# Performance work log

Measured on AMD Instinct MI355X. Metric: run time of the kernel, lower is better.

Reference implementation:

```python
import jax, jax.numpy as jnp
import numpy as np
from jax import lax

NUM_HEADS = 8
RATIO_H = 2
RATIO_W = 2


def _layer_norm(x, gamma, beta, eps=1e-5):
    mean = jnp.mean(x, axis=-1, keepdims=True)
    var = jnp.var(x, axis=-1, keepdims=True)
    return (x - mean) * lax.rsqrt(var + eps) * gamma + beta


def setup_inputs() -> dict:
    key = jax.random.key(0)
    ks = jax.random.split(key, 6)
    B, N, C = 4, 4096, 512
    std = 0.02
    return {
        "x": jax.random.normal(ks[0], (B, N, C), jnp.float32),
        "w_qkv": jax.random.normal(ks[1], (3 * C, C), jnp.float32) * std,
        "w_ke": jax.random.normal(ks[2], (C, C, RATIO_H, RATIO_W), jnp.float32) * std,
        "w_ve": jax.random.normal(ks[3], (C, C, RATIO_H, RATIO_W), jnp.float32) * std,
        "gamma_k": jnp.ones((C // NUM_HEADS,), jnp.float32),
        "beta_k": jnp.zeros((C // NUM_HEADS,), jnp.float32),
        "gamma_v": jnp.ones((C // NUM_HEADS,), jnp.float32),
        "beta_v": jnp.zeros((C // NUM_HEADS,), jnp.float32),
        "w_proj": jax.random.normal(ks[4], (C, C), jnp.float32) * std,
        "b_proj": jnp.zeros((C,), jnp.float32),
    }


def reference(x, w_qkv, w_ke, w_ve, gamma_k, beta_k, gamma_v, beta_v, w_proj, b_proj):
    B, N, C = x.shape
    H = W = int(np.sqrt(N))
    h = NUM_HEADS
    hd = C // h
    s = RATIO_H * RATIO_W
    scale = hd ** -0.5

    # qkv projection (no bias): [B, N, 3C]
    qkv = jnp.einsum('bnc,dc->bnd', x, w_qkv)
    q, k, v = jnp.split(qkv, 3, axis=-1)

    # q -> [B, h, N, hd]
    q = q.reshape(B, N, h, hd).transpose(0, 2, 1, 3)

    # spatial reduction of k, v via strided conv (kernel == stride, no bias)
    def reduce_kv(t, w):
        img = t.transpose(0, 2, 1).reshape(B, C, H, W)
        red = lax.conv_general_dilated(
            img, w, window_strides=(RATIO_H, RATIO_W), padding='VALID',
            dimension_numbers=('NCHW', 'OIHW', 'NCHW'))  # [B, C, H/rh, W/rw]
        return red.reshape(B, C, N // s).transpose(0, 2, 1).reshape(
            B, N // s, h, hd).transpose(0, 2, 1, 3)  # [B, h, N/s, hd]

    k = _layer_norm(reduce_kv(k, w_ke), gamma_k, beta_k)
    v = _layer_norm(reduce_kv(v, w_ve), gamma_v, beta_v)

    # attention: [B, h, N, N/s]
    attn = jax.nn.softmax(jnp.einsum('bhqd,bhkd->bhqk', q, k) * scale, axis=-1)
    out = jnp.einsum('bhqk,bhkd->bhqd', attn, v)  # [B, h, N, hd]
    out = out.transpose(0, 2, 1, 3).reshape(B, N, C)
    return jnp.einsum('bnc,dc->bnd', out, w_proj) + b_proj
```

## Files before the change

### kernel.cpp

```cpp
#include <hip/hip_runtime.h>
#include <hip/hip_bf16.h>

#define DEVI static __device__ __forceinline__

typedef __attribute__((ext_vector_type(4))) float f32x4;
typedef __attribute__((ext_vector_type(8))) short bf16x8;
typedef __attribute__((ext_vector_type(4))) short s16x4;
typedef __attribute__((ext_vector_type(2))) unsigned int u32x2;

DEVI unsigned short f2bf(float f) {
    union { float f; unsigned u; } v; v.f = f;
    unsigned r = v.u + 0x7fffu + ((v.u >> 16) & 1u);
    return (unsigned short)(r >> 16);
}

DEVI void gload_lds16(const void* g, void* l) {
    __builtin_amdgcn_global_load_lds(
        (const __attribute__((address_space(1))) unsigned int*)(g),
        (__attribute__((address_space(3))) unsigned int*)(l), 16, 0, 0);
}

#define EXP2A(d, x) asm("v_exp_f32 %0, %1" : "=v"(d) : "v"(x))
#define CVTPK(d, a, b) asm("v_cvt_pk_bf16_f32 %0, %1, %2" : "=v"(d) : "v"(a), "v"(b))

__global__ __launch_bounds__(256) void prep_kernel(
    const float* __restrict__ x, const float* __restrict__ w_qkv,
    const float* __restrict__ w_proj, const float* __restrict__ w_ke,
    const float* __restrict__ w_ve,
    unsigned short* __restrict__ xb, unsigned short* __restrict__ wqkvb,
    unsigned short* __restrict__ wprojb, unsigned short* __restrict__ w2k,
    unsigned short* __restrict__ w2v, unsigned short* __restrict__ wqkvT)
{
    const int blk = blockIdx.x, t = threadIdx.x;
    if (blk < 9216) {
        const float* src; unsigned short* dst; int i;
        if (blk < 8192)      { src = x;      dst = xb;     i = (blk * 256 + t) * 4; }
        else if (blk < 8960) { src = w_qkv;  dst = wqkvb;  i = ((blk - 8192) * 256 + t) * 4; }
        else                 { src = w_proj; dst = wprojb; i = ((blk - 8960) * 256 + t) * 4; }
        const float4 v = *(const float4*)(src + i);
        ushort4 o; o.x = f2bf(v.x); o.y = f2bf(v.y); o.z = f2bf(v.z); o.w = f2bf(v.w);
        *(ushort4*)(dst + i) = o;
    } else if (blk < 11264) {
        const int r = blk - 9216;
        const float* wsrc = (r < 1024) ? w_ke : w_ve;
        unsigned short* wdst = (r < 1024) ? w2k : w2v;
        const int i4 = (((r & 1023) * 256) + t) * 4;
        const int o = i4 >> 11, p = (i4 >> 9) & 3, c = i4 & 511;
        const float* s = wsrc + (o << 11) + (c << 2) + p;
        ushort4 ov; ov.x = f2bf(s[0]); ov.y = f2bf(s[4]); ov.z = f2bf(s[8]); ov.w = f2bf(s[12]);
        *(ushort4*)(wdst + i4) = ov;
    } else {
        const int r2 = blk - 11264;
        const int i4 = (r2 * 256 + t) * 4;
        const int sel = i4 >> 18;
        const int rem = i4 & 262143;
        const int d = rem >> 9, c4 = rem & 511;
        const float* s = w_qkv + (size_t)(512 + sel * 512 + c4) * 512 + d;
        ushort4 ov; ov.x = f2bf(s[0]); ov.y = f2bf(s[512]); ov.z = f2bf(s[1024]); ov.w = f2bf(s[1536]);
        *(ushort4*)(wqkvT + i4) = ov;
    }
}

template<int OUT_BF16, int ADD_BIAS>
__global__ __launch_bounds__(256) void gemm_bt(
    const unsigned short* __restrict__ A,
    const unsigned short* __restrict__ B,
    void* __restrict__ Cp, const float* __restrict__ bias,
    int N, int K)
{
    __shared__ unsigned short As[128 * 64];
    __shared__ unsigned short Bs[128 * 64];
    const int t = threadIdx.x;
    const int lane = t & 63, w = t >> 6;
    const int wr = w >> 1, wc = w & 1;
    const int lr = lane & 15, lg = lane >> 4;
    const size_t rowBase = (size_t)blockIdx.y * 128;
    const size_t colBase = (size_t)blockIdx.x * 128;

    const unsigned short* gA[4]; const unsigned short* gB[4]; int du[4];
#pragma unroll
    for (int j = 0; j < 4; ++j) {
        const int u = t * 16 + j * 4096;
        const int row = u >> 7, colb = u & 127;
        const int csw = colb ^ ((row & 7) << 4);
        du[j] = u;
        gA[j] = A + (rowBase + row) * (size_t)K + (csw >> 1);
        gB[j] = B + (colBase + row) * (size_t)K + (csw >> 1);
    }
    const int sw = (lr & 7) << 4;

    f32x4 acc[4][4] = {};

    for (int k0 = 0; k0 < K; k0 += 64) {
#pragma unroll
        for (int j = 0; j < 4; ++j) {
            gload_lds16(gA[j] + k0, (char*)As + du[j]);
            gload_lds16(gB[j] + k0, (char*)Bs + du[j]);
        }
        __syncthreads();
#pragma unroll
        for (int s = 0; s < 2; ++s) {
            const int ro = (s * 64 + lg * 16) ^ sw;
            bf16x8 af[4], bfr[4];
#pragma unroll
            for (int a = 0; a < 4; ++a)
                af[a] = *(const bf16x8*)((char*)As + (wr * 64 + a * 16 + lr) * 128 + ro);
#pragma unroll
            for (int bn = 0; bn < 4; ++bn)
                bfr[bn] = *(const bf16x8*)((char*)Bs + (wc * 64 + bn * 16 + lr) * 128 + ro);
#pragma unroll
            for (int a = 0; a < 4; ++a)
#pragma unroll
                for (int bn = 0; bn < 4; ++bn)
                    acc[a][bn] = __builtin_amdgcn_mfma_f32_16x16x32_bf16(af[a], bfr[bn], acc[a][bn], 0, 0, 0);
        }
        __syncthreads();
    }

#pragma unroll
    for (int a = 0; a < 4; ++a) {
        const size_t row = rowBase + wr * 64 + a * 16 + lg * 4;
#pragma unroll
        for (int bn = 0; bn < 4; ++bn) {
            const size_t col = colBase + wc * 64 + bn * 16 + lr;
#pragma unroll
            for (int r = 0; r < 4; ++r) {
                const float v = acc[a][bn][r];
                if (OUT_BF16) {
                    ((unsigned short*)Cp)[(row + r) * (size_t)N + col] = f2bf(v);
                } else {
                    const float vb2 = ADD_BIAS ? (v + bias[col]) : v;
                    ((float*)Cp)[(row + r) * (size_t)N + col] = vb2;
                }
            }
        }
    }
}

__global__ __launch_bounds__(256) void gemm_wt(
    const unsigned short* __restrict__ w2k,
    const unsigned short* __restrict__ w2v,
    const unsigned short* __restrict__ wqkvT,
    unsigned short* __restrict__ wtk,
    unsigned short* __restrict__ wtv)
{
    __shared__ unsigned short As[128 * 64];
    __shared__ unsigned short Bs[128 * 64];
    const int t = threadIdx.x;
    const int lane = t & 63, w = t >> 6;
    const int wr = w >> 1, wc = w & 1;
    const int lr = lane & 15, lg = lane >> 4;
    const int rowBase = blockIdx.y * 128;
    const int colBase = blockIdx.x * 128;
    const int p = blockIdx.z & 3, sel = blockIdx.z >> 2;
    const unsigned short* A = (sel ? w2v : w2k) + p * 512;
    const unsigned short* B = wqkvT + (size_t)sel * 262144;
    unsigned short* C = (sel ? wtv : wtk) + p * 512;

    const unsigned short* gA[4]; const unsigned short* gB[4]; int du[4];
#pragma unroll
    for (int j = 0; j < 4; ++j) {
        const int u = t * 16 + j * 4096;
        const int row = u >> 7, colb = u & 127;
        const int csw = colb ^ ((row & 7) << 4);
        du[j] = u;
        gA[j] = A + (size_t)(rowBase + row) * 2048 + (csw >> 1);
        gB[j] = B + (size_t)(colBase + row) * 512 + (csw >> 1);
    }
    const int sw = (lr & 7) << 4;

    f32x4 acc[4][4] = {};

    for (int k0 = 0; k0 < 512; k0 += 64) {
#pragma unroll
        for (int j = 0; j < 4; ++j) {
            gload_lds16(gA[j] + k0, (char*)As + du[j]);
            gload_lds16(gB[j] + k0, (char*)Bs + du[j]);
        }
        __syncthreads();
#pragma unroll
        for (int s = 0; s < 2; ++s) {
            const int ro = (s * 64 + lg * 16) ^ sw;
            bf16x8 af[4], bfr[4];
#pragma unroll
            for (int a = 0; a < 4; ++a)
                af[a] = *(const bf16x8*)((char*)As + (wr * 64 + a * 16 + lr) * 128 + ro);
#pragma unroll
            for (int bn = 0; bn < 4; ++bn)
                bfr[bn] = *(const bf16x8*)((char*)Bs + (wc * 64 + bn * 16 + lr) * 128 + ro);
#pragma unroll
            for (int a = 0; a < 4; ++a)
#pragma unroll
                for (int bn = 0; bn < 4; ++bn)
                    acc[a][bn] = __builtin_amdgcn_mfma_f32_16x16x32_bf16(af[a], bfr[bn], acc[a][bn], 0, 0, 0);
        }
        __syncthreads();
    }

#pragma unroll
    for (int a = 0; a < 4; ++a) {
        const size_t row = (size_t)rowBase + wr * 64 + a * 16 + lg * 4;
#pragma unroll
        for (int bn = 0; bn < 4; ++bn) {
            const size_t col = (size_t)colBase + wc * 64 + bn * 16 + lr;
#pragma unroll
            for (int r = 0; r < 4; ++r)
                C[(row + r) * 2048 + col] = f2bf(acc[a][bn][r]);
        }
    }
}

__global__ __launch_bounds__(256) void gemm_qred(
    const unsigned short* __restrict__ xb,
    const unsigned short* __restrict__ wqkvb,
    unsigned short* __restrict__ qbuf,
    const unsigned short* __restrict__ wtk,
    const unsigned short* __restrict__ wtv,
    float* __restrict__ kred)
{
    __shared__ unsigned short As[128 * 64];
    __shared__ unsigned short Bs[128 * 64];
    const int t = threadIdx.x;
    const int lane = t & 63, w = t >> 6;
    const int wr = w >> 1, wc = w & 1;
    const int lr = lane & 15, lg = lane >> 4;
    const int sw = (lr & 7) << 4;
    const int colBase = blockIdx.x * 128;

    if (blockIdx.y < 128) {
        const size_t rowBase = (size_t)blockIdx.y * 128;
        const unsigned short* gA[4]; const unsigned short* gB[4]; int du[4];
#pragma unroll
        for (int j = 0; j < 4; ++j) {
            const int u = t * 16 + j * 4096;
            const int row = u >> 7, colb = u & 127;
            const int csw = colb ^ ((row & 7) << 4);
            du[j] = u;
            gA[j] = xb + (rowBase + row) * (size_t)512 + (csw >> 1);
            gB[j] = wqkvb + (colBase + row) * (size_t)512 + (csw >> 1);
        }
        f32x4 acc[4][4] = {};
        for (int k0 = 0; k0 < 512; k0 += 64) {
#pragma unroll
            for (int j = 0; j < 4; ++j) {
                gload_lds16(gA[j] + k0, (char*)As + du[j]);
                gload_lds16(gB[j] + k0, (char*)Bs + du[j]);
            }
            __syncthreads();
#pragma unroll
            for (int s = 0; s < 2; ++s) {
                const int ro = (s * 64 + lg * 16) ^ sw;
                bf16x8 af[4], bfr[4];
#pragma unroll
                for (int a = 0; a < 4; ++a)
                    af[a] = *(const bf16x8*)((char*)As + (wr * 64 + a * 16 + lr) * 128 + ro);
#pragma unroll
                for (int bn = 0; bn < 4; ++bn)
                    bfr[bn] = *(const bf16x8*)((char*)Bs + (wc * 64 + bn * 16 + lr) * 128 + ro);
#pragma unroll
                for (int a = 0; a < 4; ++a)
#pragma unroll
                    for (int bn = 0; bn < 4; ++bn)
                        acc[a][bn] = __builtin_amdgcn_mfma_f32_16x16x32_bf16(af[a], bfr[bn], acc[a][bn], 0, 0, 0);
            }
            __syncthreads();
        }
#pragma unroll
        for (int a = 0; a < 4; ++a) {
            const size_t row = rowBase + wr * 64 + a * 16 + lg * 4;
#pragma unroll
            for (int bn = 0; bn < 4; ++bn) {
                const size_t col = (size_t)colBase + wc * 64 + bn * 16 + lr;
#pragma unroll
                for (int r = 0; r < 4; ++r)
                    qbuf[(row + r) * 512 + col] = f2bf(acc[a][bn][r]);
            }
        }
    } else {
        const int z = blockIdx.y - 128;
        const int ks = z >> 6;
        const int rowBase = (z & 63) * 128;
        const int isV = rowBase >= 4096;
        const unsigned short* Bp = isV ? wtv : wtk;

        const char* gA[4]; const unsigned short* gB[4]; int du[4];
#pragma unroll
        for (int j = 0; j < 4; ++j) {
            const int u = t * 16 + j * 4096;
            const int row = u >> 7, colb = u & 127;
            const int csw = colb ^ ((row & 7) << 4);
            du[j] = u;
            const int bm = (rowBase + row) & 4095;
            const int b = bm >> 10, m = bm & 1023;
            const int pix = (m >> 5) * 128 + (m & 31) * 2;
            gA[j] = (const char*)xb + (size_t)(b * 4096 + pix) * 1024 + csw;
            gB[j] = Bp + (colBase + row) * (size_t)2048 + (csw >> 1);
        }
        f32x4 acc[4][4] = {};
        for (int kk = 0; kk < 16; ++kk) {
            const int k0 = ks * 1024 + kk * 64;
            const int p = k0 >> 9;
            const int pd = ((p & 1) ? 1 : 0) + ((p & 2) ? 64 : 0);
            const size_t aoff = (size_t)pd * 1024 + (size_t)(k0 & 511) * 2;
#pragma unroll
            for (int j = 0; j < 4; ++j) {
                gload_lds16(gA[j] + aoff, (char*)As + du[j]);
                gload_lds16(gB[j] + k0, (char*)Bs + du[j]);
            }
            __syncthreads();
#pragma unroll
            for (int s = 0; s < 2; ++s) {
                const int ro = (s * 64 + lg * 16) ^ sw;
                bf16x8 af[4], bfr[4];
#pragma unroll
                for (int a = 0; a < 4; ++a)
                    af[a] = *(const bf16x8*)((char*)As + (wr * 64 + a * 16 + lr) * 128 + ro);
#pragma unroll
                for (int bn = 0; bn < 4; ++bn)
                    bfr[bn] = *(const bf16x8*)((char*)Bs + (wc * 64 + bn * 16 + lr) * 128 + ro);
#pragma unroll
                for (int a = 0; a < 4; ++a)
#pragma unroll
                    for (int bn = 0; bn < 4; ++bn)
                        acc[a][bn] = __builtin_amdgcn_mfma_f32_16x16x32_bf16(af[a], bfr[bn], acc[a][bn], 0, 0, 0);
            }
            __syncthreads();
        }
        float* outp = kred + (size_t)ks * 4194304;
#pragma unroll
        for (int a = 0; a < 4; ++a) {
            const size_t row = (size_t)rowBase + wr * 64 + a * 16 + lg * 4;
#pragma unroll
            for (int bn = 0; bn < 4; ++bn) {
                const size_t col = (size_t)colBase + wc * 64 + bn * 16 + lr;
#pragma unroll
                for (int r = 0; r < 4; ++r)
                    outp[(row + r) * 512 + col] = acc[a][bn][r];
            }
        }
    }
}

__global__ __launch_bounds__(256) void ln_kernel(
    const float* __restrict__ kredA, const float* __restrict__ kredB,
    const float* __restrict__ gk, const float* __restrict__ bk,
    const float* __restrict__ gv, const float* __restrict__ bv,
    unsigned short* __restrict__ outp)
{
    const int bm = blockIdx.x;
    const int sel = blockIdx.y;
    const size_t off = ((size_t)sel * 4096 + bm) * 512;
    const float* g = sel ? gv : gk;
    const float* be = sel ? bv : bk;
    const float QS = sel ? 1.0f : 0.18033688011112042f;
    unsigned short* o = outp + off;
    const int t = threadIdx.x;
    const float2 a = *(const float2*)(kredA + off + t * 2);
    const float2 b2 = *(const float2*)(kredB + off + t * 2);
    const float vx = a.x + b2.x, vy = a.y + b2.y;
    float s = vx + vy, s2 = vx * vx + vy * vy;
#pragma unroll
    for (int o2 = 1; o2 <= 16; o2 <<= 1) {
        s += __shfl_xor(s, o2);
        s2 += __shfl_xor(s2, o2);
    }
    const float mean = s * 0.015625f;
    const float var = s2 * 0.015625f - mean * mean;
    const float rstd = rsqrtf(var + 1e-5f);
    const int c = (t * 2) & 63;
    ushort2 ov;
    ov.x = f2bf(((vx - mean) * rstd * g[c] + be[c]) * QS);
    ov.y = f2bf(((vy - mean) * rstd * g[c + 1] + be[c + 1]) * QS);
    *(ushort2*)(o + t * 2) = ov;
}

__global__ __launch_bounds__(256) void transpose_v(
    const unsigned short* __restrict__ v_ln, unsigned short* __restrict__ v_t)
{
    __shared__ unsigned short tile[64][65];
    const int mb = blockIdx.x;
    const int cb = blockIdx.y;
    const int t = threadIdx.x;
#pragma unroll
    for (int i = 0; i < 16; ++i) {
        const int idx = i * 256 + t;
        const int r = idx >> 6, c = idx & 63;
        tile[r][c] = v_ln[(size_t)(mb * 64 + r) * 512 + cb * 64 + c];
    }
    __syncthreads();
    const int b = mb >> 4;
    const int mloc = (mb & 15) * 64;
#pragma unroll
    for (int i = 0; i < 16; ++i) {
        const int idx = i * 256 + t;
        const int c = idx >> 6, m = idx & 63;
        v_t[((size_t)(b * 512) + cb * 64 + c) * 1024 + mloc + m] = tile[m][c];
    }
}

__global__ __launch_bounds__(256) void attn_kernel(
    const unsigned short* __restrict__ qb,
    const unsigned short* __restrict__ k_ln,
    const unsigned short* __restrict__ v_t,
    unsigned short* __restrict__ attn_out)
{
    extern __shared__ char smem[];
    const int blk = ((blockIdx.x & 7) << 7) | (blockIdx.x >> 3);
    const int qc = blk & 31, h = (blk >> 5) & 7, b = blk >> 8;
    const int t = threadIdx.x, w = t >> 6, lane = t & 63;
    const int lr = lane & 15, lg = lane >> 4;
    const int qrow0 = qc * 128 + w * 32;

    const unsigned short* qpA = qb + (size_t)(b * 4096 + qrow0 + lr) * 512 + h * 64 + lg * 8;
    const bf16x8 qa0 = *(const bf16x8*)(qpA);
    const bf16x8 qa1 = *(const bf16x8*)(qpA + 32);
    const bf16x8 qb0 = *(const bf16x8*)(qpA + 16 * 512);
    const bf16x8 qb1 = *(const bf16x8*)(qpA + 16 * 512 + 32);

    const char* kbase = (const char*)(k_ln + (size_t)b * 524288 + h * 64);
    const char* vbase = (const char*)(v_t + ((size_t)b * 512 + h * 64) * 1024);
    const int d0 = t * 16, d1 = 4096 + t * 16;
    const int r0 = d0 >> 7, cs0 = (d0 & 127) ^ ((r0 & 7) << 4);
    const int r1 = d1 >> 7, cs1 = (d1 & 127) ^ ((r1 & 7) << 4);
    const char* gK0 = kbase + r0 * 1024 + cs0;
    const char* gK1 = kbase + r1 * 1024 + cs1;
    const char* gV0 = vbase + r0 * 2048 + cs0;
    const char* gV1 = vbase + r1 * 2048 + cs1;

#define STAGE_KV(buf, kt) do { \
    gload_lds16(gK0 + (size_t)(kt) * 65536, smem + (buf) * 8192 + d0); \
    gload_lds16(gK1 + (size_t)(kt) * 65536, smem + (buf) * 8192 + d1); \
    gload_lds16(gV0 + (kt) * 128, smem + 16384 + (buf) * 8192 + d0); \
    gload_lds16(gV1 + (kt) * 128, smem + 16384 + (buf) * 8192 + d1); \
  } while (0)

    bf16x8 ones;
#pragma unroll
    for (int i = 0; i < 8; ++i) ones[i] = (short)0x3F80;

    f32x4 accA[4] = {}, accB[4] = {};
    f32x4 psaccA = {}, psaccB = {};

    STAGE_KV(0, 0);
    __syncthreads();

    char* Pw = smem + 32768 + w * 2048;
    const int sw = (lr & 7) << 4;
    const int off0 = lr * 128 + ((lg * 16) ^ sw);
    const int off1 = lr * 128 + ((64 + lg * 16) ^ sw);
    int pwo[4];
#pragma unroll
    for (int tt = 0; tt < 4; ++tt) pwo[tt] = lr * 128 + ((tt * 32 + lg * 8) ^ sw);

#pragma unroll 2
    for (int kt = 0; kt < 16; ++kt) {
        const int cur = kt & 1;
        if (kt < 15) STAGE_KV(cur ^ 1, kt + 1);
        const char* KsB = smem + cur * 8192;
        const char* VsB = smem + 16384 + cur * 8192;

        f32x4 sa[4], sb[4];
#pragma unroll
        for (int tt = 0; tt < 4; ++tt) {
            const bf16x8 kf0 = *(const bf16x8*)(KsB + tt * 2048 + off0);
            const bf16x8 kf1 = *(const bf16x8*)(KsB + tt * 2048 + off1);
            f32x4 za = {}, zb = {};
            za = __builtin_amdgcn_mfma_f32_16x16x32_bf16(kf0, qa0, za, 0, 0, 0);
            za = __builtin_amdgcn_mfma_f32_16x16x32_bf16(kf1, qa1, za, 0, 0, 0);
            zb = __builtin_amdgcn_mfma_f32_16x16x32_bf16(kf0, qb0, zb, 0, 0, 0);
            zb = __builtin_amdgcn_mfma_f32_16x16x32_bf16(kf1, qb1, zb, 0, 0, 0);
            sa[tt] = za; sb[tt] = zb;
        }

#pragma unroll
        for (int tt = 0; tt < 4; ++tt) {
            float e0, e1, e2, e3;
            EXP2A(e0, sa[tt][0]); EXP2A(e1, sa[tt][1]);
            EXP2A(e2, sa[tt][2]); EXP2A(e3, sa[tt][3]);
            unsigned c0, c1;
            CVTPK(c0, e0, e1); CVTPK(c1, e2, e3);
            union { u32x2 u; s16x4 s; } pk; pk.u.x = c0; pk.u.y = c1;
            *(s16x4*)(Pw + pwo[tt]) = pk.s;
        }
        asm volatile("" ::: "memory");
        const bf16x8 fa0 = *(const bf16x8*)(Pw + off0);
        const bf16x8 fa1 = *(const bf16x8*)(Pw + off1);
        asm volatile("" ::: "memory");

        bf16x8 vf0[4], vf1[4];
#pragma unroll
        for (int n2 = 0; n2 < 4; ++n2) {
            vf0[n2] = *(const bf16x8*)(VsB + n2 * 2048 + off0);
            vf1[n2] = *(const bf16x8*)(VsB + n2 * 2048 + off1);
        }

#pragma unroll
        for (int n2 = 0; n2 < 4; ++n2) {
            accA[n2] = __builtin_amdgcn_mfma_f32_16x16x32_bf16(fa0, vf0[n2], accA[n2], 0, 0, 0);
            accA[n2] = __builtin_amdgcn_mfma_f32_16x16x32_bf16(fa1, vf1[n2], accA[n2], 0, 0, 0);
        }
        psaccA = __builtin_amdgcn_mfma_f32_16x16x32_bf16(fa0, ones, psaccA, 0, 0, 0);
        psaccA = __builtin_amdgcn_mfma_f32_16x16x32_bf16(fa1, ones, psaccA, 0, 0, 0);

#pragma unroll
        for (int tt = 0; tt < 4; ++tt) {
            float e0, e1, e2, e3;
            EXP2A(e0, sb[tt][0]); EXP2A(e1, sb[tt][1]);
            EXP2A(e2, sb[tt][2]); EXP2A(e3, sb[tt][3]);
            unsigned c0, c1;
            CVTPK(c0, e0, e1); CVTPK(c1, e2, e3);
            union { u32x2 u; s16x4 s; } pk; pk.u.x = c0; pk.u.y = c1;
            *(s16x4*)(Pw + pwo[tt]) = pk.s;
        }
        asm volatile("" ::: "memory");
        const bf16x8 fb0 = *(const bf16x8*)(Pw + off0);
        const bf16x8 fb1 = *(const bf16x8*)(Pw + off1);

#pragma unroll
        for (int n2 = 0; n2 < 4; ++n2) {
            accB[n2] = __builtin_amdgcn_mfma_f32_16x16x32_bf16(fb0, vf0[n2], accB[n2], 0, 0, 0);
            accB[n2] = __builtin_amdgcn_mfma_f32_16x16x32_bf16(fb1, vf1[n2], accB[n2], 0, 0, 0);
        }
        psaccB = __builtin_amdgcn_mfma_f32_16x16x32_bf16(fb0, ones, psaccB, 0, 0, 0);
        psaccB = __builtin_amdgcn_mfma_f32_16x16x32_bf16(fb1, ones, psaccB, 0, 0, 0);
        __syncthreads();
    }
#undef STAGE_KV

    float dA[4], dB[4];
#pragma unroll
    for (int r = 0; r < 4; ++r) {
        dA[r] = 1.0f / psaccA[r];
        dB[r] = 1.0f / psaccB[r];
    }
    unsigned short* oA = attn_out + (size_t)(b * 4096 + qrow0 + lg * 4) * 512 + h * 64;
#pragma unroll
    for (int n2 = 0; n2 < 4; ++n2)
#pragma unroll
        for (int r = 0; r < 4; ++r) {
            oA[(size_t)r * 512 + n2 * 16 + lr] = f2bf(accA[n2][r] * dA[r]);
            oA[(size_t)(16 + r) * 512 + n2 * 16 + lr] = f2bf(accB[n2][r] * dB[r]);
        }
}

extern "C" void kernel_launch(void* const* d_in, const int* in_sizes, int n_in,
                              void* d_out, int out_size, void* d_ws, size_t ws_size,
                              hipStream_t stream)
{
    (void)in_sizes; (void)n_in; (void)out_size; (void)ws_size;
    const float* x       = (const float*)d_in[0];
    const float* w_qkv   = (const float*)d_in[1];
    const float* w_ke    = (const float*)d_in[2];
    const float* w_ve    = (const float*)d_in[3];
    const float* gamma_k = (const float*)d_in[4];
    const float* beta_k  = (const float*)d_in[5];
    const float* gamma_v = (const float*)d_in[6];
    const float* beta_v  = (const float*)d_in[7];
    const float* w_proj  = (const float*)d_in[8];
    const float* b_proj  = (const float*)d_in[9];
    float* out = (float*)d_out;

    char* ws = (char*)d_ws;
    unsigned short* qb     = (unsigned short*)(ws + 0);
    unsigned short* wtk    = (unsigned short*)(ws + 16777216);
    unsigned short* wtv    = (unsigned short*)(ws + 18874368);
    unsigned short* wqkvT  = (unsigned short*)(ws + 20971520);
    unsigned short* xb     = (unsigned short*)(ws + 50331648);
    unsigned short* attn_o = xb;
    float*          kredB  = (float*)(ws + 67108864);
    float*          kredA  = (float*)(ws + 83886080);
    unsigned short* k_ln   = (unsigned short*)(ws + 100663296);
    unsigned short* v_ln   = (unsigned short*)(ws + 104857600);
    unsigned short* v_t    = (unsigned short*)(ws + 109051904);
    unsigned short* wqkvb  = (unsigned short*)(ws + 113246208);
    unsigned short* w2k    = (unsigned short*)(ws + 114819072);
    unsigned short* w2v    = (unsigned short*)(ws + 116916224);
    unsigned short* wprojb = (unsigned short*)(ws + 119013376);

    prep_kernel<<<11776, 256, 0, stream>>>(x, w_qkv, w_proj, w_ke, w_ve,
                                           xb, wqkvb, wprojb, w2k, w2v, wqkvT);

    gemm_wt<<<dim3(4, 4, 8), 256, 0, stream>>>(w2k, w2v, wqkvT, wtk, wtv);

    gemm_qred<<<dim3(4, 256), 256, 0, stream>>>(xb, wqkvb, qb, wtk, wtv, kredB);

    ln_kernel<<<dim3(4096, 2), 256, 0, stream>>>(kredA, kredB,
                                                 gamma_k, beta_k, gamma_v, beta_v, k_ln);

    transpose_v<<<dim3(64, 8), 256, 0, stream>>>(v_ln, v_t);

    attn_kernel<<<1024, 256, 40960, stream>>>(qb, k_ln, v_t, attn_o);

    gemm_bt<0, 1><<<dim3(4, 128), 256, 0, stream>>>(
        attn_o, wprojb, out, b_proj, 512, 512);
}
```

Measured before the change: 141.5 us.

## Fuse V layernorm into transpose and shrink projection GEMM row tile

The V half of the layernorm is folded into the transpose kernel. Each 4-thread group normalizes one head row in registers and writes bf16 straight into the transpose tile, so the v_ln intermediate is never written to or read back from global memory. Separately, the output projection GEMM drops from 128-row to 64-row tiles, doubling the block count to 1024 so more blocks are available across CUs. The cost is more redundant B-tile loads per output element in the projection GEMM.

```diff
diff --git a/kernel.cpp b/kernel.cpp
--- a/kernel.cpp
+++ b/kernel.cpp
@@ -61,82 +61,6 @@
     }
 }
 
-template<int OUT_BF16, int ADD_BIAS>
-__global__ __launch_bounds__(256) void gemm_bt(
-    const unsigned short* __restrict__ A,
-    const unsigned short* __restrict__ B,
-    void* __restrict__ Cp, const float* __restrict__ bias,
-    int N, int K)
-{
-    __shared__ unsigned short As[128 * 64];
-    __shared__ unsigned short Bs[128 * 64];
-    const int t = threadIdx.x;
-    const int lane = t & 63, w = t >> 6;
-    const int wr = w >> 1, wc = w & 1;
-    const int lr = lane & 15, lg = lane >> 4;
-    const size_t rowBase = (size_t)blockIdx.y * 128;
-    const size_t colBase = (size_t)blockIdx.x * 128;
-
-    const unsigned short* gA[4]; const unsigned short* gB[4]; int du[4];
-#pragma unroll
-    for (int j = 0; j < 4; ++j) {
-        const int u = t * 16 + j * 4096;
-        const int row = u >> 7, colb = u & 127;
-        const int csw = colb ^ ((row & 7) << 4);
-        du[j] = u;
-        gA[j] = A + (rowBase + row) * (size_t)K + (csw >> 1);
-        gB[j] = B + (colBase + row) * (size_t)K + (csw >> 1);
-    }
-    const int sw = (lr & 7) << 4;
-
-    f32x4 acc[4][4] = {};
-
-    for (int k0 = 0; k0 < K; k0 += 64) {
-#pragma unroll
-        for (int j = 0; j < 4; ++j) {
-            gload_lds16(gA[j] + k0, (char*)As + du[j]);
-            gload_lds16(gB[j] + k0, (char*)Bs + du[j]);
-        }
-        __syncthreads();
-#pragma unroll
-        for (int s = 0; s < 2; ++s) {
-            const int ro = (s * 64 + lg * 16) ^ sw;
-            bf16x8 af[4], bfr[4];
-#pragma unroll
-            for (int a = 0; a < 4; ++a)
-                af[a] = *(const bf16x8*)((char*)As + (wr * 64 + a * 16 + lr) * 128 + ro);
-#pragma unroll
-            for (int bn = 0; bn < 4; ++bn)
-                bfr[bn] = *(const bf16x8*)((char*)Bs + (wc * 64 + bn * 16 + lr) * 128 + ro);
-#pragma unroll
-            for (int a = 0; a < 4; ++a)
-#pragma unroll
-                for (int bn = 0; bn < 4; ++bn)
-                    acc[a][bn] = __builtin_amdgcn_mfma_f32_16x16x32_bf16(af[a], bfr[bn], acc[a][bn], 0, 0, 0);
-        }
-        __syncthreads();
-    }
-
-#pragma unroll
-    for (int a = 0; a < 4; ++a) {
-        const size_t row = rowBase + wr * 64 + a * 16 + lg * 4;
-#pragma unroll
-        for (int bn = 0; bn < 4; ++bn) {
-            const size_t col = colBase + wc * 64 + bn * 16 + lr;
-#pragma unroll
-            for (int r = 0; r < 4; ++r) {
-                const float v = acc[a][bn][r];
-                if (OUT_BF16) {
-                    ((unsigned short*)Cp)[(row + r) * (size_t)N + col] = f2bf(v);
-                } else {
-                    const float vb2 = ADD_BIAS ? (v + bias[col]) : v;
-                    ((float*)Cp)[(row + r) * (size_t)N + col] = vb2;
-                }
-            }
-        }
-    }
-}
-
 __global__ __launch_bounds__(256) void gemm_wt(
     const unsigned short* __restrict__ w2k,
     const unsigned short* __restrict__ w2v,
@@ -344,15 +268,11 @@
 __global__ __launch_bounds__(256) void ln_kernel(
     const float* __restrict__ kredA, const float* __restrict__ kredB,
     const float* __restrict__ gk, const float* __restrict__ bk,
-    const float* __restrict__ gv, const float* __restrict__ bv,
     unsigned short* __restrict__ outp)
 {
     const int bm = blockIdx.x;
-    const int sel = blockIdx.y;
-    const size_t off = ((size_t)sel * 4096 + bm) * 512;
-    const float* g = sel ? gv : gk;
-    const float* be = sel ? bv : bk;
-    const float QS = sel ? 1.0f : 0.18033688011112042f;
+    const size_t off = (size_t)bm * 512;
+    const float QS = 0.18033688011112042f;
     unsigned short* o = outp + off;
     const int t = threadIdx.x;
     const float2 a = *(const float2*)(kredA + off + t * 2);
@@ -369,23 +289,43 @@
     const float rstd = rsqrtf(var + 1e-5f);
     const int c = (t * 2) & 63;
     ushort2 ov;
-    ov.x = f2bf(((vx - mean) * rstd * g[c] + be[c]) * QS);
-    ov.y = f2bf(((vy - mean) * rstd * g[c + 1] + be[c + 1]) * QS);
+    ov.x = f2bf(((vx - mean) * rstd * gk[c] + bk[c]) * QS);
+    ov.y = f2bf(((vy - mean) * rstd * gk[c + 1] + bk[c + 1]) * QS);
     *(ushort2*)(o + t * 2) = ov;
 }
 
-__global__ __launch_bounds__(256) void transpose_v(
-    const unsigned short* __restrict__ v_ln, unsigned short* __restrict__ v_t)
+__global__ __launch_bounds__(256) void lnt_v(
+    const float* __restrict__ kredA, const float* __restrict__ kredB,
+    const float* __restrict__ gv, const float* __restrict__ bv,
+    unsigned short* __restrict__ v_t)
 {
     __shared__ unsigned short tile[64][65];
     const int mb = blockIdx.x;
     const int cb = blockIdx.y;
     const int t = threadIdx.x;
+    const int r = t >> 2, qt = t & 3;
+
+    const size_t base = ((size_t)(4096 + mb * 64 + r)) * 512 + cb * 64 + qt * 16;
+    float v[16];
+    float s = 0.f, s2 = 0.f;
+#pragma unroll
+    for (int i = 0; i < 4; ++i) {
+        const float4 a = *(const float4*)(kredA + base + i * 4);
+        const float4 b2 = *(const float4*)(kredB + base + i * 4);
+        const float e0 = a.x + b2.x, e1 = a.y + b2.y, e2 = a.z + b2.z, e3 = a.w + b2.w;
+        v[i * 4 + 0] = e0; v[i * 4 + 1] = e1; v[i * 4 + 2] = e2; v[i * 4 + 3] = e3;
+        s += (e0 + e1) + (e2 + e3);
+        s2 += (e0 * e0 + e1 * e1) + (e2 * e2 + e3 * e3);
+    }
+    s += __shfl_xor(s, 1); s += __shfl_xor(s, 2);
+    s2 += __shfl_xor(s2, 1); s2 += __shfl_xor(s2, 2);
+    const float mean = s * 0.015625f;
+    const float var = s2 * 0.015625f - mean * mean;
+    const float rstd = rsqrtf(var + 1e-5f);
 #pragma unroll
     for (int i = 0; i < 16; ++i) {
-        const int idx = i * 256 + t;
-        const int r = idx >> 6, c = idx & 63;
-        tile[r][c] = v_ln[(size_t)(mb * 64 + r) * 512 + cb * 64 + c];
+        const int c = qt * 16 + i;
+        tile[r][c] = f2bf((v[i] - mean) * rstd * gv[c] + bv[c]);
     }
     __syncthreads();
     const int b = mb >> 4;
@@ -395,6 +335,81 @@
         const int idx = i * 256 + t;
         const int c = idx >> 6, m = idx & 63;
         v_t[((size_t)(b * 512) + cb * 64 + c) * 1024 + mloc + m] = tile[m][c];
+    }
+}
+
+__global__ __launch_bounds__(256) void gemm_proj(
+    const unsigned short* __restrict__ A,
+    const unsigned short* __restrict__ B,
+    float* __restrict__ C, const float* __restrict__ bias)
+{
+    __shared__ unsigned short As[64 * 64];
+    __shared__ unsigned short Bs[128 * 64];
+    const int t = threadIdx.x;
+    const int lane = t & 63, w = t >> 6;
+    const int wr = w >> 1, wc = w & 1;
+    const int lr = lane & 15, lg = lane >> 4;
+    const size_t rowBase = (size_t)blockIdx.y * 64;
+    const size_t colBase = (size_t)blockIdx.x * 128;
+
+    const unsigned short* gA[2]; const unsigned short* gB[4]; int duA[2], duB[4];
+#pragma unroll
+    for (int j = 0; j < 2; ++j) {
+        const int u = t * 16 + j * 4096;
+        const int row = u >> 7, colb = u & 127;
+        const int csw = colb ^ ((row & 7) << 4);
+        duA[j] = u;
+        gA[j] = A + (rowBase + row) * (size_t)512 + (csw >> 1);
+    }
+#pragma unroll
+    for (int j = 0; j < 4; ++j) {
+        const int u = t * 16 + j * 4096;
+        const int row = u >> 7, colb = u & 127;
+        const int csw = colb ^ ((row & 7) << 4);
+        duB[j] = u;
+        gB[j] = B + (colBase + row) * (size_t)512 + (csw >> 1);
+    }
+    const int sw = (lr & 7) << 4;
+
+    f32x4 acc[2][4] = {};
+
+    for (int k0 = 0; k0 < 512; k0 += 64) {
+#pragma unroll
+        for (int j = 0; j < 2; ++j)
+            gload_lds16(gA[j] + k0, (char*)As + duA[j]);
+#pragma unroll
+        for (int j = 0; j < 4; ++j)
+            gload_lds16(gB[j] + k0, (char*)Bs + duB[j]);
+        __syncthreads();
+#pragma unroll
+        for (int s = 0; s < 2; ++s) {
+            const int ro = (s * 64 + lg * 16) ^ sw;
+            bf16x8 af[2], bfr[4];
+#pragma unroll
+            for (int a = 0; a < 2; ++a)
+                af[a] = *(const bf16x8*)((char*)As + (wr * 32 + a * 16 + lr) * 128 + ro);
+#pragma unroll
+            for (int bn = 0; bn < 4; ++bn)
+                bfr[bn] = *(const bf16x8*)((char*)Bs + (wc * 64 + bn * 16 + lr) * 128 + ro);
+#pragma unroll
+            for (int a = 0; a < 2; ++a)
+#pragma unroll
+                for (int bn = 0; bn < 4; ++bn)
+                    acc[a][bn] = __builtin_amdgcn_mfma_f32_16x16x32_bf16(af[a], bfr[bn], acc[a][bn], 0, 0, 0);
+        }
+        __syncthreads();
+    }
+
+#pragma unroll
+    for (int a = 0; a < 2; ++a) {
+        const size_t row = rowBase + wr * 32 + a * 16 + lg * 4;
+#pragma unroll
+        for (int bn = 0; bn < 4; ++bn) {
+            const size_t col = colBase + wc * 64 + bn * 16 + lr;
+#pragma unroll
+            for (int r = 0; r < 4; ++r)
+                C[(row + r) * 512 + col] = acc[a][bn][r] + bias[col];
+        }
     }
 }
 
@@ -570,7 +585,6 @@
     float*          kredB  = (float*)(ws + 67108864);
     float*          kredA  = (float*)(ws + 83886080);
     unsigned short* k_ln   = (unsigned short*)(ws + 100663296);
-    unsigned short* v_ln   = (unsigned short*)(ws + 104857600);
     unsigned short* v_t    = (unsigned short*)(ws + 109051904);
     unsigned short* wqkvb  = (unsigned short*)(ws + 113246208);
     unsigned short* w2k    = (unsigned short*)(ws + 114819072);
@@ -584,13 +598,11 @@
 
     gemm_qred<<<dim3(4, 256), 256, 0, stream>>>(xb, wqkvb, qb, wtk, wtv, kredB);
 
-    ln_kernel<<<dim3(4096, 2), 256, 0, stream>>>(kredA, kredB,
-                                                 gamma_k, beta_k, gamma_v, beta_v, k_ln);
-
-    transpose_v<<<dim3(64, 8), 256, 0, stream>>>(v_ln, v_t);
+    ln_kernel<<<4096, 256, 0, stream>>>(kredA, kredB, gamma_k, beta_k, k_ln);
+
+    lnt_v<<<dim3(64, 8), 256, 0, stream>>>(kredA, kredB, gamma_v, beta_v, v_t);
 
     attn_kernel<<<1024, 256, 40960, stream>>>(qb, k_ln, v_t, attn_o);
 
-    gemm_bt<0, 1><<<dim3(4, 128), 256, 0, stream>>>(
-        attn_o, wprojb, out, b_proj, 512, 512);
-}
+    gemm_proj<<<dim3(4, 256), 256, 0, stream>>>(attn_o, wprojb, out, b_proj);
+}
```

Result: no change. 140.5 us (-0.7%).
